# Performance work log

Measured on AMD Instinct MI355X. Metric: run time of the kernel, lower is better.

## Reference

```python
import jax, jax.numpy as jnp
import numpy as np

# Standard JPEG luminance quantization table, transposed as in the original DiffJPEG repo.
_Y_TABLE = np.array([
    [16, 11, 10, 16, 24, 40, 51, 61],
    [12, 12, 14, 19, 26, 58, 60, 55],
    [14, 13, 16, 24, 40, 57, 69, 56],
    [14, 17, 22, 29, 51, 87, 80, 62],
    [18, 22, 37, 56, 68, 109, 103, 77],
    [24, 35, 55, 64, 81, 104, 113, 92],
    [49, 64, 78, 87, 103, 121, 120, 101],
    [72, 92, 95, 98, 112, 100, 103, 99]], dtype=np.float32).T

_n = np.arange(8)
_C = np.cos((2 * _n[:, None] + 1) * _n[None, :] * np.pi / 16)  # [spatial, freq]
_DCT_T = (_C[:, None, :, None] * _C[None, :, None, :]).astype(np.float32)
# IDCT basis: tensor[x,y,u,v] = cos((2u+1)x pi/16) cos((2v+1)y pi/16) (contract over x,y = freq)
_IDCT_T = (_C.T[:, None, :, None] * _C.T[None, :, None, :]).astype(np.float32)
_alpha = np.array([1.0 / np.sqrt(2)] + [1.0] * 7, dtype=np.float32)
_SCALE = (np.outer(_alpha, _alpha) * 0.25).astype(np.float32)   # DCT scale
_ALPHA = np.outer(_alpha, _alpha).astype(np.float32)            # IDCT alpha

_QUALITY = 80.0
_FACTOR = (200.0 - _QUALITY * 2) / 100.0  # = 0.4 (quality >= 50 branch)


def _diff_round(x):
    r = jnp.round(x)
    return r + (x - r) ** 3


def setup_inputs() -> dict:
    key = jax.random.key(0)
    x = jax.random.uniform(key, (8, 3, 1024, 1024), dtype=jnp.float32)
    return {"x": x}


def reference(x):
    k = 8
    B, C, H, W = x.shape
    y_tab = jnp.asarray(_Y_TABLE) * _FACTOR
    dct_t = jnp.asarray(_DCT_T)
    idct_t = jnp.asarray(_IDCT_T)
    scale = jnp.asarray(_SCALE)
    alpha = jnp.asarray(_ALPHA)

    img = x * 255.0
    # Block split: [B,C,H,W] -> [B,C,nblocks,8,8] (row-major block order, as torch code)
    blocks = img.reshape(B, C, H // k, k, W // k, k)
    blocks = blocks.transpose(0, 1, 2, 4, 3, 5).reshape(B, C, -1, k, k)

    # DCT (note: this repo applies y_table quantization to all 3 channels)
    dct = scale * jnp.einsum('bcnxy,xyuv->bcnuv', blocks - 128.0, dct_t)
    q = _diff_round(dct / y_tab)
    y, cb, cr = q[:, 0], q[:, 1], q[:, 2]

    # Dequantize + IDCT
    deq = q * y_tab
    sp = 0.25 * jnp.einsum('bcnuv,uvxy->bcnxy', deq * alpha, idct_t) + 128.0

    # Block merge back to [B,C,H,W]
    rec = sp.reshape(B, C, H // k, W // k, k, k)
    rec = rec.transpose(0, 1, 2, 4, 3, 5).reshape(B, C, H, W)
    rec = jnp.clip(rec, 0.0, 255.0) / 255.0
    return (y, cb, cr, rec)
```

## Files before the change

kernel.cpp:

```cpp
#include <hip/hip_runtime.h>
#include <cstddef>

#define CD1 0.9807852804032304
#define CD2 0.9238795325112867
#define CD3 0.8314696123025452
#define CD4 0.7071067811865476
#define CD5 0.5555702330196022
#define CD6 0.3826834323650898
#define CD7 0.19509032201612825

__device__ const int YLg[64] = {
  16,11,10,16,24,40,51,61,
  12,12,14,19,26,58,60,55,
  14,13,16,24,40,57,69,56,
  14,17,22,29,51,87,80,62,
  18,22,37,56,68,109,103,77,
  24,35,55,64,81,104,113,92,
  49,64,78,87,103,121,120,101,
  72,92,95,98,112,100,103,99
};

__global__ __launch_bounds__(256) void diffjpeg_kernel(const float* __restrict__ in,
                                                       float* __restrict__ out)
{
    __shared__ float lds[4480];

    const float CT[8][8] = {
      {1.0f,(float)CD1,(float)CD2,(float)CD3,(float)CD4,(float)CD5,(float)CD6,(float)CD7},
      {1.0f,(float)CD3,(float)CD6,(float)(-CD7),(float)(-CD4),(float)(-CD1),(float)(-CD2),(float)(-CD5)},
      {1.0f,(float)CD5,(float)(-CD6),(float)(-CD1),(float)(-CD4),(float)CD7,(float)CD2,(float)CD3},
      {1.0f,(float)CD7,(float)(-CD2),(float)(-CD5),(float)CD4,(float)CD3,(float)(-CD6),(float)(-CD1)},
      {1.0f,(float)(-CD7),(float)(-CD2),(float)CD5,(float)CD4,(float)(-CD3),(float)(-CD6),(float)CD1},
      {1.0f,(float)(-CD5),(float)(-CD6),(float)CD1,(float)(-CD4),(float)(-CD7),(float)CD2,(float)(-CD3)},
      {1.0f,(float)(-CD3),(float)CD6,(float)CD7,(float)(-CD4),(float)CD1,(float)(-CD2),(float)CD5},
      {1.0f,(float)(-CD1),(float)CD2,(float)(-CD3),(float)CD4,(float)(-CD5),(float)CD6,(float)(-CD7)}
    };

    const int tid = threadIdx.x;
    const int wg  = blockIdx.x;
    const int bc  = wg >> 9;
    const int rem = wg & 511;
    const int bh  = rem >> 2;
    const int bwq = (rem & 3) * 32;
    const int ch  = bc % 3;
    const int bb  = bc / 3;

    const int blk = tid >> 3;
    const int p   = tid & 7;

    const size_t ibase = (size_t)bc * 1048576 + (size_t)bh * 8192 + (size_t)bwq * 8;

    float d1[8];
    {
        const float* src = in + ibase + (size_t)p * 1024 + blk * 8;
        const float4 m0 = *reinterpret_cast<const float4*>(src);
        const float4 m1 = *reinterpret_cast<const float4*>(src + 4);
        float s[8] = {m0.x, m0.y, m0.z, m0.w, m1.x, m1.y, m1.z, m1.w};
#pragma unroll
        for (int y = 0; y < 8; ++y) s[y] = fmaf(s[y], 255.0f, -128.0f);
#pragma unroll
        for (int v = 0; v < 8; ++v) {
            float acc = 0.0f;
#pragma unroll
            for (int y = 0; y < 8; ++y) acc = fmaf(s[y], CT[y][v], acc);
            d1[v] = acc;
        }
    }

    if (tid < 64) {
        const int u = tid >> 3, v = tid & 7;
        const double a_u = u ? 1.0 : 0.7071067811865476;
        const double a_v = v ? 1.0 : 0.7071067811865476;
        const double qt  = (double)YLg[v * 8 + u] * 0.4;
        const double al  = a_u * a_v;
        lds[4352 + tid] = (float)(al * 0.25 / qt);
        lds[4416 + tid] = (float)(qt * al * 0.25);
    }

    *reinterpret_cast<float4*>(&lds[blk * 68 + p * 8])     = make_float4(d1[0], d1[1], d1[2], d1[3]);
    *reinterpret_cast<float4*>(&lds[blk * 68 + p * 8 + 4]) = make_float4(d1[4], d1[5], d1[6], d1[7]);
    __syncthreads();

    {
        float c0[8];
#pragma unroll
        for (int x = 0; x < 8; ++x) c0[x] = lds[blk * 68 + x * 8 + p];
        float dq[8];
#pragma unroll
        for (int u = 0; u < 8; ++u) {
            float acc = 0.0f;
#pragma unroll
            for (int x = 0; x < 8; ++x) acc = fmaf(CT[x][u], c0[x], acc);
            const float kq = lds[4352 + u * 8 + p];
            const float kd = lds[4416 + u * 8 + p];
            const float xq = acc * kq;
            const float r  = rintf(xq);
            const float d  = xq - r;
            const float qv = r + d * d * d;
            lds[2176 + blk * 68 + u * 8 + p] = qv;
            dq[u] = qv * kd;
        }
#pragma unroll
        for (int x = 0; x < 8; ++x) {
            float acc = 0.0f;
#pragma unroll
            for (int u = 0; u < 8; ++u) acc = fmaf(CT[x][u], dq[u], acc);
            lds[blk * 68 + x * 8 + p] = acc;
        }
    }
    __syncthreads();

    {
        float* qb = out + (size_t)ch * 8388608 + (size_t)bb * 1048576
                        + ((size_t)(bh * 128) + bwq) * 64;
#pragma unroll
        for (int j = 0; j < 2; ++j) {
            const int flat = j * 1024 + tid * 4;
            const int rec = flat >> 6, off = flat & 63;
            const float4 val = *reinterpret_cast<const float4*>(&lds[2176 + rec * 68 + off]);
            *reinterpret_cast<float4*>(qb + flat) = val;
        }
    }

    {
        const float4 a0 = *reinterpret_cast<const float4*>(&lds[blk * 68 + p * 8]);
        const float4 a1 = *reinterpret_cast<const float4*>(&lds[blk * 68 + p * 8 + 4]);
        const float e[8] = {a0.x, a0.y, a0.z, a0.w, a1.x, a1.y, a1.z, a1.w};
        float orow[8];
#pragma unroll
        for (int y = 0; y < 8; ++y) {
            float acc = 0.0f;
#pragma unroll
            for (int v = 0; v < 8; ++v) acc = fmaf(e[v], CT[y][v], acc);
            acc += 128.0f;
            acc = fminf(fmaxf(acc, 0.0f), 255.0f);
            orow[y] = acc * (1.0f / 255.0f);
        }
        float* rb = out + (size_t)25165824 + ibase + (size_t)p * 1024 + blk * 8;
        *reinterpret_cast<float4*>(rb)     = make_float4(orow[0], orow[1], orow[2], orow[3]);
        *reinterpret_cast<float4*>(rb + 4) = make_float4(orow[4], orow[5], orow[6], orow[7]);
    }
}

extern "C" void kernel_launch(void* const* d_in, const int* in_sizes, int n_in,
                              void* d_out, int out_size, void* d_ws, size_t ws_size,
                              hipStream_t stream) {
    const float* x = (const float*)d_in[0];
    float*       o = (float*)d_out;
    diffjpeg_kernel<<<12288, 256, 0, stream>>>(x, o);
}
```

Baseline: 58.10 us.

## Shrink workgroups to one wave, precompute quant tables, stage output through LDS

Each workgroup now handles 8 blocks with 64 threads instead of 32 blocks with 256 threads, and launches 4x as many workgroups. The quantization and dequantization tables are computed at compile time into a constant device array and loaded per thread, instead of being built in LDS with double-precision math every launch. The reconstructed image is transposed through LDS so each row of 64 floats is written contiguously, and all outputs use nontemporal stores. The goal is to cut setup overhead and improve write coalescing, at the cost of an extra barrier and more, smaller workgroups.

```diff
diff --git a/kernel.cpp b/kernel.cpp
--- a/kernel.cpp
+++ b/kernel.cpp
@@ -9,21 +9,37 @@
 #define CD6 0.3826834323650898
 #define CD7 0.19509032201612825
 
-__device__ const int YLg[64] = {
-  16,11,10,16,24,40,51,61,
-  12,12,14,19,26,58,60,55,
-  14,13,16,24,40,57,69,56,
-  14,17,22,29,51,87,80,62,
-  18,22,37,56,68,109,103,77,
-  24,35,55,64,81,104,113,92,
-  49,64,78,87,103,121,120,101,
-  72,92,95,98,112,100,103,99
-};
+typedef float v4f __attribute__((ext_vector_type(4)));
 
-__global__ __launch_bounds__(256) void diffjpeg_kernel(const float* __restrict__ in,
-                                                       float* __restrict__ out)
+struct Tabs { float kq[64]; float kd[64]; };
+constexpr Tabs mk_tabs() {
+    Tabs t{};
+    constexpr int YL[64] = {
+      16,11,10,16,24,40,51,61,
+      12,12,14,19,26,58,60,55,
+      14,13,16,24,40,57,69,56,
+      14,17,22,29,51,87,80,62,
+      18,22,37,56,68,109,103,77,
+      24,35,55,64,81,104,113,92,
+      49,64,78,87,103,121,120,101,
+      72,92,95,98,112,100,103,99 };
+    for (int p = 0; p < 8; ++p)
+      for (int u = 0; u < 8; ++u) {
+        const double a_u = u ? 1.0 : 0.7071067811865476;
+        const double a_p = p ? 1.0 : 0.7071067811865476;
+        const double qt  = (double)YL[p * 8 + u] * 0.4;
+        const double al  = a_u * a_p;
+        t.kq[p * 8 + u] = (float)(al * 0.25 / qt);
+        t.kd[p * 8 + u] = (float)(qt * al * 0.25);
+      }
+    return t;
+}
+__device__ const Tabs TB = mk_tabs();
+
+__global__ __launch_bounds__(64) void diffjpeg_kernel(const float* __restrict__ in,
+                                                      float* __restrict__ out)
 {
-    __shared__ float lds[4480];
+    __shared__ float lds[1632];
 
     const float CT[8][8] = {
       {1.0f,(float)CD1,(float)CD2,(float)CD3,(float)CD4,(float)CD5,(float)CD6,(float)CD7},
@@ -38,24 +54,31 @@
 
     const int tid = threadIdx.x;
     const int wg  = blockIdx.x;
-    const int bc  = wg >> 9;
-    const int rem = wg & 511;
-    const int bh  = rem >> 2;
-    const int bwq = (rem & 3) * 32;
+    const int bc  = wg >> 11;
+    const int rem = wg & 2047;
+    const int bh  = rem >> 4;
+    const int wq  = rem & 15;
     const int ch  = bc % 3;
     const int bb  = bc / 3;
 
     const int blk = tid >> 3;
     const int p   = tid & 7;
 
-    const size_t ibase = (size_t)bc * 1048576 + (size_t)bh * 8192 + (size_t)bwq * 8;
+    const size_t ibase = (size_t)bc * 1048576 + (size_t)bh * 8192 + (size_t)wq * 64;
 
-    float d1[8];
+    const v4f kq0 = *reinterpret_cast<const v4f*>(&TB.kq[p * 8]);
+    const v4f kq1 = *reinterpret_cast<const v4f*>(&TB.kq[p * 8 + 4]);
+    const v4f kd0 = *reinterpret_cast<const v4f*>(&TB.kd[p * 8]);
+    const v4f kd1 = *reinterpret_cast<const v4f*>(&TB.kd[p * 8 + 4]);
+    const float kq[8] = {kq0.x,kq0.y,kq0.z,kq0.w,kq1.x,kq1.y,kq1.z,kq1.w};
+    const float kd[8] = {kd0.x,kd0.y,kd0.z,kd0.w,kd1.x,kd1.y,kd1.z,kd1.w};
+
     {
         const float* src = in + ibase + (size_t)p * 1024 + blk * 8;
         const float4 m0 = *reinterpret_cast<const float4*>(src);
         const float4 m1 = *reinterpret_cast<const float4*>(src + 4);
         float s[8] = {m0.x, m0.y, m0.z, m0.w, m1.x, m1.y, m1.z, m1.w};
+        float d1[8];
 #pragma unroll
         for (int y = 0; y < 8; ++y) s[y] = fmaf(s[y], 255.0f, -128.0f);
 #pragma unroll
@@ -65,20 +88,9 @@
             for (int y = 0; y < 8; ++y) acc = fmaf(s[y], CT[y][v], acc);
             d1[v] = acc;
         }
+        *reinterpret_cast<float4*>(&lds[blk * 68 + p * 8])     = make_float4(d1[0], d1[1], d1[2], d1[3]);
+        *reinterpret_cast<float4*>(&lds[blk * 68 + p * 8 + 4]) = make_float4(d1[4], d1[5], d1[6], d1[7]);
     }
-
-    if (tid < 64) {
-        const int u = tid >> 3, v = tid & 7;
-        const double a_u = u ? 1.0 : 0.7071067811865476;
-        const double a_v = v ? 1.0 : 0.7071067811865476;
-        const double qt  = (double)YLg[v * 8 + u] * 0.4;
-        const double al  = a_u * a_v;
-        lds[4352 + tid] = (float)(al * 0.25 / qt);
-        lds[4416 + tid] = (float)(qt * al * 0.25);
-    }
-
-    *reinterpret_cast<float4*>(&lds[blk * 68 + p * 8])     = make_float4(d1[0], d1[1], d1[2], d1[3]);
-    *reinterpret_cast<float4*>(&lds[blk * 68 + p * 8 + 4]) = make_float4(d1[4], d1[5], d1[6], d1[7]);
     __syncthreads();
 
     {
@@ -91,14 +103,12 @@
             float acc = 0.0f;
 #pragma unroll
             for (int x = 0; x < 8; ++x) acc = fmaf(CT[x][u], c0[x], acc);
-            const float kq = lds[4352 + u * 8 + p];
-            const float kd = lds[4416 + u * 8 + p];
-            const float xq = acc * kq;
+            const float xq = acc * kq[u];
             const float r  = rintf(xq);
             const float d  = xq - r;
             const float qv = r + d * d * d;
-            lds[2176 + blk * 68 + u * 8 + p] = qv;
-            dq[u] = qv * kd;
+            lds[544 + blk * 68 + u * 8 + p] = qv;
+            dq[u] = qv * kd[u];
         }
 #pragma unroll
         for (int x = 0; x < 8; ++x) {
@@ -112,13 +122,13 @@
 
     {
         float* qb = out + (size_t)ch * 8388608 + (size_t)bb * 1048576
-                        + ((size_t)(bh * 128) + bwq) * 64;
+                        + ((size_t)(bh * 128) + wq * 8) * 64;
 #pragma unroll
         for (int j = 0; j < 2; ++j) {
-            const int flat = j * 1024 + tid * 4;
+            const int flat = j * 256 + tid * 4;
             const int rec = flat >> 6, off = flat & 63;
-            const float4 val = *reinterpret_cast<const float4*>(&lds[2176 + rec * 68 + off]);
-            *reinterpret_cast<float4*>(qb + flat) = val;
+            const v4f val = *reinterpret_cast<const v4f*>(&lds[544 + rec * 68 + off]);
+            __builtin_nontemporal_store(val, reinterpret_cast<v4f*>(qb + flat));
         }
     }
 
@@ -136,9 +146,20 @@
             acc = fminf(fmaxf(acc, 0.0f), 255.0f);
             orow[y] = acc * (1.0f / 255.0f);
         }
-        float* rb = out + (size_t)25165824 + ibase + (size_t)p * 1024 + blk * 8;
-        *reinterpret_cast<float4*>(rb)     = make_float4(orow[0], orow[1], orow[2], orow[3]);
-        *reinterpret_cast<float4*>(rb + 4) = make_float4(orow[4], orow[5], orow[6], orow[7]);
+        *reinterpret_cast<float4*>(&lds[1088 + p * 68 + blk * 8])     = make_float4(orow[0], orow[1], orow[2], orow[3]);
+        *reinterpret_cast<float4*>(&lds[1088 + p * 68 + blk * 8 + 4]) = make_float4(orow[4], orow[5], orow[6], orow[7]);
+    }
+    __syncthreads();
+
+    {
+        float* rb = out + (size_t)25165824 + ibase;
+#pragma unroll
+        for (int j = 0; j < 2; ++j) {
+            const int flat = j * 256 + tid * 4;
+            const int r = flat >> 6, c = flat & 63;
+            const v4f val = *reinterpret_cast<const v4f*>(&lds[1088 + r * 68 + c]);
+            __builtin_nontemporal_store(val, reinterpret_cast<v4f*>(rb + (size_t)r * 1024 + c));
+        }
     }
 }
 
@@ -147,5 +168,5 @@
                               hipStream_t stream) {
     const float* x = (const float*)d_in[0];
     float*       o = (float*)d_out;
-    diffjpeg_kernel<<<12288, 256, 0, stream>>>(x, o);
+    diffjpeg_kernel<<<49152, 64, 0, stream>>>(x, o);
 }
```

Result: faster. 49.10 us (-15.5%).
